# Performance work log

Hardware: AMD Instinct MI355X
Metric: run time of the kernel (lower is better)

The kernel has to match this reference:

```python
import jax, jax.numpy as jnp
import numpy as np

D_MODEL = 1024
D_STATE = 16
D_CONV = 4
D_INNER = 2 * D_MODEL          # expand * d_model
DT_RANK = (D_MODEL + 15) // 16 # ceil(d_model/16) = 64
BATCH, SEQLEN = 2, 1024


def setup_inputs() -> dict:
    key = jax.random.key(0)
    ks = jax.random.split(key, 8)
    s = lambda k, shape, scale=0.02: (jax.random.normal(k, shape, jnp.float32) * scale)
    return {
        "hidden_states": jax.random.normal(ks[0], (BATCH, SEQLEN, D_MODEL), jnp.float32),
        "in_proj_w": s(ks[1], (2 * D_INNER, D_MODEL)),
        "conv_w": s(ks[2], (D_INNER, 1, D_CONV), 0.3),   # depthwise conv kernel (O, I/groups=1, K)
        "conv_b": jnp.zeros((D_INNER,), jnp.float32),
        "x_proj_w": s(ks[3], (DT_RANK + 2 * D_STATE, D_INNER)),
        "dt_proj_w": s(ks[4], (D_INNER, DT_RANK), 0.1),
        # inverse-softplus of small dt values, like the torch init
        "dt_proj_b": jax.random.uniform(ks[5], (D_INNER,), jnp.float32, minval=-5.0, maxval=-2.0),
        "A_log": jnp.log(jnp.broadcast_to(jnp.arange(1, D_STATE + 1, dtype=jnp.float32), (D_INNER, D_STATE))),
        "D": jnp.ones((D_INNER,), jnp.float32),
        "out_proj_w": s(ks[6], (D_MODEL, D_INNER)),
    }


def _forward(hidden_states, in_proj_w, conv_w, conv_b, x_proj_w,
             dt_proj_w, dt_proj_b, A_log, D, out_proj_w):
    B, L, _ = hidden_states.shape
    # in_proj -> split into x, z
    xz = hidden_states @ in_proj_w.T                      # [B, L, 2*d_inner]
    x, z = jnp.split(xz, 2, axis=-1)
    # causal depthwise conv1d (pad left d_conv-1, then take first L) + SiLU
    xc = jnp.transpose(x, (0, 2, 1))                      # [B, d_inner, L]
    xc = jax.lax.conv_general_dilated(
        xc, conv_w, window_strides=(1,), padding=[(D_CONV - 1, 0)],
        feature_group_count=D_INNER,
        dimension_numbers=("NCH", "OIH", "NCH")) + conv_b[None, :, None]
    xc = jax.nn.silu(xc)
    u = jnp.transpose(xc, (0, 2, 1)).astype(jnp.float32)  # [B, L, d_inner]
    # x_proj -> dt_low, B, C
    x_dbl = u @ x_proj_w.T                                # [B, L, dt_rank + 2*d_state]
    dt_low, Bp, Cp = jnp.split(x_dbl, [DT_RANK, DT_RANK + D_STATE], axis=-1)
    dt = dt_low @ dt_proj_w.T + dt_proj_b                 # [B, L, d_inner]
    # NOTE: original adds dt_proj.bias AGAIN as delta_bias inside the scan, then softplus
    delta = jax.nn.softplus(dt + dt_proj_b)
    A = -jnp.exp(A_log.astype(jnp.float32))               # [d_inner, d_state]
    # discretization
    dA = jnp.exp(jnp.einsum("bld,dn->lbdn", delta, A))    # [L, B, d, n]
    dBu = jnp.einsum("bld,bln,bld->lbdn", delta, Bp.astype(jnp.float32), u)
    C_t = jnp.transpose(Cp.astype(jnp.float32), (1, 0, 2))  # [L, B, n]

    def step(state, inp):
        a, b, c = inp
        state = a * state + b                             # [B, d, n]
        y = jnp.einsum("bdn,bn->bd", state, c)
        return state, y

    x0 = jnp.zeros((B, D_INNER, D_STATE), jnp.float32)
    _, ys = jax.lax.scan(step, x0, (dA, dBu, C_t))        # ys: [L, B, d]
    y = jnp.transpose(ys, (1, 0, 2))                      # [B, L, d]
    y = y + u * D.astype(jnp.float32)                     # skip connection
    y = y * jax.nn.silu(z.astype(jnp.float32))            # gating
    y = y.astype(hidden_states.dtype)
    return y @ out_proj_w.T                               # [B, L, d_model]


def reference(hidden_states, in_proj_w, conv_w, conv_b, x_proj_w,
              dt_proj_w, dt_proj_b, A_log, D, out_proj_w):
    return _forward(hidden_states, in_proj_w, conv_w, conv_b, x_proj_w,
                    dt_proj_w, dt_proj_b, A_log, D, out_proj_w)
```

## Files before the change

### kernel.cpp

```cpp
#include <hip/hip_runtime.h>
#include <hip/hip_bf16.h>
#include <math.h>

#define BATCH   2
#define SEQLEN  1024
#define DMODEL  1024
#define DINNER  2048
#define DSTATE  16
#define DTRANK  64
#define XPAD    128
#define MROWS   (BATCH*SEQLEN)
#define NSEG    8
#define SEGLEN  (SEQLEN/NSEG)
#define XP_SPLIT  8

typedef float    f32x4  __attribute__((ext_vector_type(4)));
typedef _Float16 f16x8  __attribute__((ext_vector_type(8)));
typedef _Float16 f16x4  __attribute__((ext_vector_type(4)));

template<int EPI>
__global__ __launch_bounds__(256) void pgemm64(
    const _Float16* __restrict__ A, int lda,
    const _Float16* __restrict__ W, int ldw,
    float* __restrict__ C, int ldc, int K,
    const float* __restrict__ bias, _Float16* __restrict__ C16, size_t zstride)
{
  constexpr int APS = 520;
  constexpr int BPS = 1032;
  __shared__ _Float16 As[2][8 * APS];
  __shared__ _Float16 Bs[2][8 * BPS];

  const int t  = threadIdx.x;
  const int m0 = blockIdx.y * 64, n0 = blockIdx.x * 128;
  const int kchunk = K / gridDim.z;
  const int kbeg = blockIdx.z * kchunk;
  const int nIter = kchunk / 64;

  const int kb = t & 7;
  const int r0 = t >> 3;
  const _Float16* gA = A + (size_t)(m0 + r0) * lda + kbeg + kb * 8;
  const _Float16* gB = W + (size_t)(n0 + r0) * ldw + kbeg + kb * 8;
  const size_t a32 = (size_t)32 * lda;
  const size_t b32 = (size_t)32 * ldw;
  const int aoff = kb * APS + r0 * 8;
  const int boff = kb * BPS + r0 * 8;

  {
    f16x8 a0 = *(const f16x8*)(gA);
    f16x8 a1 = *(const f16x8*)(gA + a32);
    f16x8 b0 = *(const f16x8*)(gB);
    f16x8 b1 = *(const f16x8*)(gB + b32);
    f16x8 b2 = *(const f16x8*)(gB + 2 * b32);
    f16x8 b3 = *(const f16x8*)(gB + 3 * b32);
    gA += 64; gB += 64;
    *(f16x8*)&As[0][aoff]       = a0;
    *(f16x8*)&As[0][aoff + 256] = a1;
    *(f16x8*)&Bs[0][boff]       = b0;
    *(f16x8*)&Bs[0][boff + 256] = b1;
    *(f16x8*)&Bs[0][boff + 512] = b2;
    *(f16x8*)&Bs[0][boff + 768] = b3;
  }

  const int lane = t & 63, wvi = t >> 6;
  const int wn = wvi * 32;
  const int lm = lane & 15, lk = lane >> 4;

  f32x4 acc[4][2] = {};

  for (int it = 0; it < nIter; ++it) {
    __syncthreads();
    const bool more = (it + 1 < nIter);
    f16x8 a0, a1, b0, b1, b2, b3;
    if (more) {
      a0 = *(const f16x8*)(gA);
      a1 = *(const f16x8*)(gA + a32);
      b0 = *(const f16x8*)(gB);
      b1 = *(const f16x8*)(gB + b32);
      b2 = *(const f16x8*)(gB + 2 * b32);
      b3 = *(const f16x8*)(gB + 3 * b32);
      gA += 64; gB += 64;
    }
    const int cb = it & 1;
#pragma unroll
    for (int s = 0; s < 2; ++s) {
      f16x8 av[4], bv[2];
#pragma unroll
      for (int i = 0; i < 4; ++i)
        av[i] = *(const f16x8*)&As[cb][(s * 4 + lk) * APS + (i * 16 + lm) * 8];
#pragma unroll
      for (int j = 0; j < 2; ++j)
        bv[j] = *(const f16x8*)&Bs[cb][(s * 4 + lk) * BPS + (wn + j * 16 + lm) * 8];
#pragma unroll
      for (int i = 0; i < 4; ++i)
#pragma unroll
        for (int j = 0; j < 2; ++j)
          acc[i][j] = __builtin_amdgcn_mfma_f32_16x16x32_f16(av[i], bv[j], acc[i][j], 0, 0, 0);
    }
    if (more) {
      const int nb = (it + 1) & 1;
      *(f16x8*)&As[nb][aoff]       = a0;
      *(f16x8*)&As[nb][aoff + 256] = a1;
      *(f16x8*)&Bs[nb][boff]       = b0;
      *(f16x8*)&Bs[nb][boff + 256] = b1;
      *(f16x8*)&Bs[nb][boff + 512] = b2;
      *(f16x8*)&Bs[nb][boff + 768] = b3;
    }
  }

  float* Cz = C + (size_t)blockIdx.z * zstride;
#pragma unroll
  for (int i = 0; i < 4; ++i) {
    const int mrow = m0 + i * 16 + lk * 4;
#pragma unroll
    for (int j = 0; j < 2; ++j) {
      const int col = n0 + wn + j * 16 + lm;
#pragma unroll
      for (int r = 0; r < 4; ++r) {
        float v = acc[i][j][r];
        size_t off = (size_t)(mrow + r) * ldc + col;
        if constexpr (EPI == 0) {
          Cz[off] = v;
        } else {
          float x = v + 2.f * bias[col];
          float sp = (x > 20.f) ? x : log1pf(__expf(x));
          C16[off] = (_Float16)sp;
        }
      }
    }
  }
}

template<int EPI>
__global__ __launch_bounds__(256) void pgemm128(
    const _Float16* __restrict__ A, int lda,
    const _Float16* __restrict__ W, int ldw,
    float* __restrict__ C, int ldc, int K,
    _Float16* __restrict__ C16)
{
  constexpr int PS = 1032;
  __shared__ _Float16 As[2][8 * PS];
  __shared__ _Float16 Bs[2][8 * PS];

  const int t  = threadIdx.x;
  const int m0 = blockIdx.y * 128, n0 = blockIdx.x * 128;
  const int nIter = K / 64;

  const int kb = t & 7;
  const int r0 = t >> 3;
  const _Float16* gA = A + (size_t)(m0 + r0) * lda + kb * 8;
  const _Float16* gB = W + (size_t)(n0 + r0) * ldw + kb * 8;
  const size_t a32 = (size_t)32 * lda;
  const size_t b32 = (size_t)32 * ldw;
  const int soff = kb * PS + r0 * 8;

  {
    f16x8 ar[4], br[4];
#pragma unroll
    for (int j = 0; j < 4; ++j) {
      ar[j] = *(const f16x8*)(gA + j * a32);
      br[j] = *(const f16x8*)(gB + j * b32);
    }
    gA += 64; gB += 64;
#pragma unroll
    for (int j = 0; j < 4; ++j) {
      *(f16x8*)&As[0][soff + j * 256] = ar[j];
      *(f16x8*)&Bs[0][soff + j * 256] = br[j];
    }
  }

  const int lane = t & 63, wvi = t >> 6;
  const int wm = (wvi >> 1) * 64, wn = (wvi & 1) * 64;
  const int lm = lane & 15, lk = lane >> 4;

  f32x4 acc[4][4] = {};

  for (int it = 0; it < nIter; ++it) {
    __syncthreads();
    const bool more = (it + 1 < nIter);
    f16x8 ar[4], br[4];
    if (more) {
#pragma unroll
      for (int j = 0; j < 4; ++j) {
        ar[j] = *(const f16x8*)(gA + j * a32);
        br[j] = *(const f16x8*)(gB + j * b32);
      }
      gA += 64; gB += 64;
    }
    const int cb = it & 1;
#pragma unroll
    for (int s = 0; s < 2; ++s) {
      f16x8 av[4], bv[4];
#pragma unroll
      for (int i = 0; i < 4; ++i)
        av[i] = *(const f16x8*)&As[cb][(s * 4 + lk) * PS + (wm + i * 16 + lm) * 8];
#pragma unroll
      for (int j = 0; j < 4; ++j)
        bv[j] = *(const f16x8*)&Bs[cb][(s * 4 + lk) * PS + (wn + j * 16 + lm) * 8];
#pragma unroll
      for (int i = 0; i < 4; ++i)
#pragma unroll
        for (int j = 0; j < 4; ++j)
          acc[i][j] = __builtin_amdgcn_mfma_f32_16x16x32_f16(av[i], bv[j], acc[i][j], 0, 0, 0);
    }
    if (more) {
      const int nb = (it + 1) & 1;
#pragma unroll
      for (int j = 0; j < 4; ++j) {
        *(f16x8*)&As[nb][soff + j * 256] = ar[j];
        *(f16x8*)&Bs[nb][soff + j * 256] = br[j];
      }
    }
  }

#pragma unroll
  for (int i = 0; i < 4; ++i) {
    const int mrow = m0 + wm + i * 16 + lk * 4;
#pragma unroll
    for (int j = 0; j < 4; ++j) {
      const int col = n0 + wn + j * 16 + lm;
#pragma unroll
      for (int r = 0; r < 4; ++r) {
        float v = acc[i][j][r];
        size_t off = (size_t)(mrow + r) * ldc + col;
        if constexpr (EPI == 0) {
          C[off] = v;
        } else {
          C16[off] = (_Float16)v;
        }
      }
    }
  }
}

#define R0 (MROWS * DMODEL / 4)
#define R1 (2 * DINNER * DMODEL / 4)
#define R2 (DMODEL * DINNER / 4)
#define R3 (DINNER * DTRANK / 4)
#define R4 (XPAD * DINNER / 4)
#define F2H_TOTAL (R0 + R1 + R2 + R3 + R4)

__global__ __launch_bounds__(256) void f2h_all(
    const float* __restrict__ hid, const float* __restrict__ w_in,
    const float* __restrict__ w_out, const float* __restrict__ w_dt,
    const float* __restrict__ w_xp,
    _Float16* __restrict__ hid16, _Float16* __restrict__ w_in16,
    _Float16* __restrict__ w_out16, _Float16* __restrict__ w_dt16,
    _Float16* __restrict__ w_xp16)
{
  int i = blockIdx.x * 256 + threadIdx.x;
  const float* src; _Float16* dst; int off;
  if (i < R0)                     { src = hid;   dst = hid16;   off = i; }
  else if (i < R0+R1)             { src = w_in;  dst = w_in16;  off = i - R0; }
  else if (i < R0+R1+R2)          { src = w_out; dst = w_out16; off = i - (R0+R1); }
  else if (i < R0+R1+R2+R3)       { src = w_dt;  dst = w_dt16;  off = i - (R0+R1+R2); }
  else if (i < F2H_TOTAL) {
    off = i - (R0+R1+R2+R3);
    int r = (off * 4) >> 11;
    f16x4 h = {0, 0, 0, 0};
    if (r < 96) {
      float4 v = ((const float4*)w_xp)[off];
      h = (f16x4){(_Float16)v.x, (_Float16)v.y, (_Float16)v.z, (_Float16)v.w};
    }
    ((f16x4*)w_xp16)[off] = h;
    return;
  } else return;
  float4 v = ((const float4*)src)[off];
  ((f16x4*)dst)[off] = (f16x4){(_Float16)v.x, (_Float16)v.y, (_Float16)v.z, (_Float16)v.w};
}

__global__ __launch_bounds__(256) void reduce_xdbl(
    const float* __restrict__ part,
    float* __restrict__ xdbl32, _Float16* __restrict__ xdbl16)
{
  int i = blockIdx.x * 256 + threadIdx.x;
  f32x4 s = ((const f32x4*)part)[i];
#pragma unroll
  for (int z = 1; z < XP_SPLIT; ++z)
    s += ((const f32x4*)part)[(size_t)z * (MROWS * XPAD / 4) + i];
  ((f32x4*)xdbl32)[i] = s;
  int col4 = (i & 31) * 4;
  if (col4 < DTRANK) {
    int row = i >> 5;
    *(f16x4*)&xdbl16[(size_t)row * DTRANK + col4] =
        (f16x4){(_Float16)s.x, (_Float16)s.y, (_Float16)s.z, (_Float16)s.w};
  }
}

__global__ __launch_bounds__(256) void conv_silu(
    const _Float16* __restrict__ xz16,
    const float* __restrict__ conv_w,
    const float* __restrict__ conv_b,
    _Float16* __restrict__ u16)
{
  const int idx = blockIdx.x * 256 + threadIdx.x;
  const int d   = idx & (DINNER - 1);
  const int row = idx >> 11;
  const int l   = row & (SEQLEN - 1);
  float s = conv_b[d];
#pragma unroll
  for (int k = 0; k < 4; ++k) {
    int lt = l + k - 3;
    if (lt >= 0)
      s = fmaf((float)xz16[(size_t)(row + k - 3) * (2 * DINNER) + d],
               conv_w[d * 4 + k], s);
  }
  float v = s / (1.f + __expf(-s));
  u16[idx] = (_Float16)v;
}

__device__ __forceinline__ float row_sum16(float x) {
  int v = __builtin_bit_cast(int, x);
  x += __builtin_bit_cast(float, __builtin_amdgcn_update_dpp(0, v, 0x128, 0xF, 0xF, true));
  v = __builtin_bit_cast(int, x);
  x += __builtin_bit_cast(float, __builtin_amdgcn_update_dpp(0, v, 0x124, 0xF, 0xF, true));
  v = __builtin_bit_cast(int, x);
  x += __builtin_bit_cast(float, __builtin_amdgcn_update_dpp(0, v, 0x4E, 0xF, 0xF, true));
  v = __builtin_bit_cast(int, x);
  x += __builtin_bit_cast(float, __builtin_amdgcn_update_dpp(0, v, 0xB1, 0xF, 0xF, true));
  return x;
}

__global__ __launch_bounds__(256) void scan_part1(
    const _Float16* __restrict__ delta16,
    const _Float16* __restrict__ u16,
    const float* __restrict__ x_dbl,
    const float* __restrict__ A_log,
    float* __restrict__ pbuf, float* __restrict__ ebuf)
{
  const int t = threadIdx.x;
  const int c = t >> 4, n = t & 15;
  const int bb = blockIdx.x;
  const int seg = bb >> 8;
  const int r = bb & 255;
  const int b = r >> 7;
  const int d_base = (r & 127) * 16;

  const float A_dn = -__expf(A_log[(d_base + c) * DSTATE + n]);
  float s = 0.f, p = 1.f;

  __shared__ __align__(16) float dl[16 * 68];
  __shared__ __align__(16) float ul[16 * 68];
  __shared__ __align__(16) float Bl[16 * 68];

  const int i_st = t >> 2;
  const int cc = (t & 3) * 4;

  for (int l0 = seg * SEGLEN; l0 < seg * SEGLEN + SEGLEN; l0 += 64) {
    const int row = b * SEQLEN + l0 + i_st;
    {
      f16x4  dh = *(const f16x4*)&delta16[(size_t)row * DINNER + d_base + cc];
      f16x4  uh = *(const f16x4*)&u16[(size_t)row * DINNER + d_base + cc];
      float4 Bv = *(const float4*)&x_dbl[(size_t)row * XPAD + DTRANK + cc];
      dl[(cc+0)*68 + i_st] = (float)dh[0]; dl[(cc+1)*68 + i_st] = (float)dh[1];
      dl[(cc+2)*68 + i_st] = (float)dh[2]; dl[(cc+3)*68 + i_st] = (float)dh[3];
      ul[(cc+0)*68 + i_st] = (float)uh[0]; ul[(cc+1)*68 + i_st] = (float)uh[1];
      ul[(cc+2)*68 + i_st] = (float)uh[2]; ul[(cc+3)*68 + i_st] = (float)uh[3];
      Bl[(cc+0)*68 + i_st] = Bv.x; Bl[(cc+1)*68 + i_st] = Bv.y;
      Bl[(cc+2)*68 + i_st] = Bv.z; Bl[(cc+3)*68 + i_st] = Bv.w;
    }
    __syncthreads();
#pragma unroll
    for (int i0 = 0; i0 < 64; i0 += 4) {
      f32x4 dv4 = *(const f32x4*)&dl[c * 68 + i0];
      f32x4 uv4 = *(const f32x4*)&ul[c * 68 + i0];
      f32x4 Bv4 = *(const f32x4*)&Bl[n * 68 + i0];
#pragma unroll
      for (int rr = 0; rr < 4; ++rr) {
        float dA = __expf(dv4[rr] * A_dn);
        s = fmaf(dA, s, dv4[rr] * Bv4[rr] * uv4[rr]);
        p *= dA;
      }
    }
    __syncthreads();
  }
  const int peIdx = (r * NSEG + seg) * 256 + t;
  pbuf[peIdx] = p;
  ebuf[peIdx] = s;
}

__global__ __launch_bounds__(256) void scan_part2(
    const _Float16* __restrict__ delta16,
    const _Float16* __restrict__ u16,
    const _Float16* __restrict__ xz16,
    const float* __restrict__ x_dbl,
    const float* __restrict__ A_log,
    const float* __restrict__ Dp,
    const float* __restrict__ pbuf,
    const float* __restrict__ ebuf,
    _Float16* __restrict__ y16)
{
  const int t = threadIdx.x;
  const int c = t >> 4, n = t & 15;
  const int bb = blockIdx.x;
  const int seg = bb >> 8;
  const int r = bb & 255;
  const int b = r >> 7;
  const int d_base = (r & 127) * 16;

  const float A_dn = -__expf(A_log[(d_base + c) * DSTATE + n]);

  float s = 0.f;
  {
    const int base = r * NSEG * 256 + t;
    for (int k = 0; k < seg; ++k)
      s = fmaf(pbuf[base + k * 256], s, ebuf[base + k * 256]);
  }

  __shared__ __align__(16) float dl[16 * 68];
  __shared__ __align__(16) float ul[16 * 68];
  __shared__ __align__(16) float Bl[16 * 68];
  __shared__ __align__(16) float Cl[16 * 68];
  __shared__ __align__(16) float yl[16 * 68];
  __shared__ __align__(16) float z_s[64 * 16];
  __shared__ float Dp_s[16];

  if (t < 16) Dp_s[t] = Dp[d_base + t];

  const int i_st = t >> 2;
  const int cc = (t & 3) * 4;

  for (int l0 = seg * SEGLEN; l0 < seg * SEGLEN + SEGLEN; l0 += 64) {
    const int row = b * SEQLEN + l0 + i_st;
    {
      f16x4  dh = *(const f16x4*)&delta16[(size_t)row * DINNER + d_base + cc];
      f16x4  uh = *(const f16x4*)&u16[(size_t)row * DINNER + d_base + cc];
      float4 Bv = *(const float4*)&x_dbl[(size_t)row * XPAD + DTRANK + cc];
      float4 Cv = *(const float4*)&x_dbl[(size_t)row * XPAD + DTRANK + DSTATE + cc];
      f16x4  zh = *(const f16x4*)&xz16[(size_t)row * (2 * DINNER) + DINNER + d_base + cc];
      dl[(cc+0)*68 + i_st] = (float)dh[0]; dl[(cc+1)*68 + i_st] = (float)dh[1];
      dl[(cc+2)*68 + i_st] = (float)dh[2]; dl[(cc+3)*68 + i_st] = (float)dh[3];
      ul[(cc+0)*68 + i_st] = (float)uh[0]; ul[(cc+1)*68 + i_st] = (float)uh[1];
      ul[(cc+2)*68 + i_st] = (float)uh[2]; ul[(cc+3)*68 + i_st] = (float)uh[3];
      Bl[(cc+0)*68 + i_st] = Bv.x; Bl[(cc+1)*68 + i_st] = Bv.y;
      Bl[(cc+2)*68 + i_st] = Bv.z; Bl[(cc+3)*68 + i_st] = Bv.w;
      Cl[(cc+0)*68 + i_st] = Cv.x; Cl[(cc+1)*68 + i_st] = Cv.y;
      Cl[(cc+2)*68 + i_st] = Cv.z; Cl[(cc+3)*68 + i_st] = Cv.w;
      float4 zv = make_float4((float)zh[0], (float)zh[1], (float)zh[2], (float)zh[3]);
      *(float4*)&z_s[t * 4] = zv;
    }
    __syncthreads();

#pragma unroll
    for (int i0 = 0; i0 < 64; i0 += 4) {
      f32x4 dv4 = *(const f32x4*)&dl[c * 68 + i0];
      f32x4 uv4 = *(const f32x4*)&ul[c * 68 + i0];
      f32x4 Bv4 = *(const f32x4*)&Bl[n * 68 + i0];
      f32x4 Cv4 = *(const f32x4*)&Cl[n * 68 + i0];
      f32x4 py;
#pragma unroll
      for (int rr = 0; rr < 4; ++rr) {
        float dA = __expf(dv4[rr] * A_dn);
        s = fmaf(dA, s, dv4[rr] * Bv4[rr] * uv4[rr]);
        py[rr] = row_sum16(s * Cv4[rr]);
      }
      if (n == 0) *(f32x4*)&yl[c * 68 + i0] = py;
    }
    __syncthreads();

#pragma unroll
    for (int k = 0; k < 4; ++k) {
      int o = t + 256 * k;
      int i = o >> 4, c2 = o & 15;
      float ssum = yl[c2 * 68 + i];
      float uv = ul[c2 * 68 + i];
      float zv = z_s[o];
      float yv = fmaf(uv, Dp_s[c2], ssum);
      yv *= zv / (1.f + __expf(-zv));
      y16[(size_t)(b * SEQLEN + l0 + i) * DINNER + d_base + c2] = (_Float16)yv;
    }
    __syncthreads();
  }
}

extern "C" void kernel_launch(void* const* d_in, const int* in_sizes, int n_in,
                              void* d_out, int out_size, void* d_ws, size_t ws_size,
                              hipStream_t stream)
{
  const float* hidden     = (const float*)d_in[0];
  const float* in_proj_w  = (const float*)d_in[1];
  const float* conv_w     = (const float*)d_in[2];
  const float* conv_b     = (const float*)d_in[3];
  const float* x_proj_w   = (const float*)d_in[4];
  const float* dt_proj_w  = (const float*)d_in[5];
  const float* dt_proj_b  = (const float*)d_in[6];
  const float* A_log      = (const float*)d_in[7];
  const float* Dp         = (const float*)d_in[8];
  const float* out_proj_w = (const float*)d_in[9];
  float* out = (float*)d_out;

  char* p = (char*)d_ws;
  _Float16* xz16    = (_Float16*)p;  p += (size_t)MROWS * 2 * DINNER * 2;
  _Float16* u16     = (_Float16*)p;  p += (size_t)MROWS * DINNER * 2;
  float*    xdbl32  = (float*)p;     p += (size_t)MROWS * XPAD * 4;
  _Float16* delta16 = (_Float16*)p;  p += (size_t)MROWS * DINNER * 2;
  _Float16* h16     = (_Float16*)p;  p += (size_t)MROWS * DMODEL * 2;
  _Float16* win16   = (_Float16*)p;  p += (size_t)2 * DINNER * DMODEL * 2;
  _Float16* wout16  = (_Float16*)p;  p += (size_t)DMODEL * DINNER * 2;
  _Float16* wdt16   = (_Float16*)p;  p += (size_t)DINNER * DTRANK * 2;
  _Float16* wxp16   = (_Float16*)p;  p += (size_t)XPAD * DINNER * 2;
  _Float16* xdbl16  = (_Float16*)p;  p += (size_t)MROWS * DTRANK * 2;
  _Float16* y16     = (_Float16*)p;  p += (size_t)MROWS * DINNER * 2;
  float*    pbuf    = (float*)p;     p += (size_t)256 * NSEG * 256 * 4;
  float*    ebuf    = (float*)p;     p += (size_t)256 * NSEG * 256 * 4;
  float*    xp_part = (float*)delta16;

  f2h_all<<<(F2H_TOTAL + 255) / 256, 256, 0, stream>>>(
      hidden, in_proj_w, out_proj_w, dt_proj_w, x_proj_w,
      h16, win16, wout16, wdt16, wxp16);

  pgemm128<4><<<dim3(4096 / 128, MROWS / 128, 1), 256, 0, stream>>>(
      h16, DMODEL, win16, DMODEL, nullptr, 4096, DMODEL, xz16);

  conv_silu<<<(MROWS * DINNER) / 256, 256, 0, stream>>>(xz16, conv_w, conv_b, u16);

  pgemm64<0><<<dim3(1, MROWS / 64, XP_SPLIT), 256, 0, stream>>>(
      u16, DINNER, wxp16, DINNER, xp_part, XPAD, DINNER, nullptr, nullptr,
      (size_t)MROWS * XPAD);

  reduce_xdbl<<<(MROWS * XPAD / 4) / 256, 256, 0, stream>>>(xp_part, xdbl32, xdbl16);

  pgemm64<2><<<dim3(DINNER / 128, MROWS / 64, 1), 256, 0, stream>>>(
      xdbl16, DTRANK, wdt16, DTRANK, nullptr, DINNER, DTRANK, dt_proj_b, delta16, 0);

  scan_part1<<<256 * NSEG, 256, 0, stream>>>(delta16, u16, xdbl32, A_log, pbuf, ebuf);
  scan_part2<<<256 * NSEG, 256, 0, stream>>>(delta16, u16, xz16, xdbl32, A_log, Dp,
                                             pbuf, ebuf, y16);

  pgemm64<0><<<dim3(DMODEL / 128, MROWS / 64, 1), 256, 0, stream>>>(
      y16, DINNER, wout16, DINNER, out, DMODEL, DINNER, nullptr, nullptr, 0);
}
```

Before: 244.1 us.

## Fuse causal conv and SiLU into x_proj GEMM and scan loaders

Removes the standalone conv_silu kernel and the u16 intermediate buffer. The depthwise causal conv plus SiLU is now recomputed from xz16 inside the x_proj GEMM's A-tile loader and inside both scan kernels' shared-memory staging. This saves one launch and a write and reread of an 8 MB activation. In exchange, each consumer reads four shifted rows of xz16 and recomputes exp, so global reads and ALU work triple, and the GEMM's A loads become slower.

After: 255.7 us. +4.8%, slower.

```diff
diff --git a/kernel.cpp b/kernel.cpp
--- a/kernel.cpp
+++ b/kernel.cpp
@@ -18,12 +18,40 @@
 typedef _Float16 f16x8  __attribute__((ext_vector_type(8)));
 typedef _Float16 f16x4  __attribute__((ext_vector_type(4)));
 
-template<int EPI>
+__device__ __forceinline__ f16x8 conv_row8(
+    const _Float16* __restrict__ xz, int mrow, int dbase,
+    const float* __restrict__ conv_w, const float* __restrict__ conv_b)
+{
+  const int l = mrow & (SEQLEN - 1);
+  const _Float16* base = xz + (size_t)mrow * (2 * DINNER) + dbase;
+  float acc[8];
+#pragma unroll
+  for (int j = 0; j < 8; ++j) acc[j] = conv_b[dbase + j];
+#pragma unroll
+  for (int k = 0; k < 4; ++k) {
+    if (l + k - 3 >= 0) {
+      f16x8 xh = *(const f16x8*)(base + (ptrdiff_t)(k - 3) * (2 * DINNER));
+#pragma unroll
+      for (int j = 0; j < 8; ++j)
+        acc[j] = fmaf((float)xh[j], conv_w[(dbase + j) * 4 + k], acc[j]);
+    }
+  }
+  f16x8 r;
+#pragma unroll
+  for (int j = 0; j < 8; ++j) {
+    float s = acc[j];
+    r[j] = (_Float16)(s / (1.f + __expf(-s)));
+  }
+  return r;
+}
+
+template<int EPI, bool CONVA>
 __global__ __launch_bounds__(256) void pgemm64(
     const _Float16* __restrict__ A, int lda,
     const _Float16* __restrict__ W, int ldw,
     float* __restrict__ C, int ldc, int K,
-    const float* __restrict__ bias, _Float16* __restrict__ C16, size_t zstride)
+    const float* __restrict__ bias, _Float16* __restrict__ C16, size_t zstride,
+    const float* __restrict__ conv_w, const float* __restrict__ conv_b)
 {
   constexpr int APS = 520;
   constexpr int BPS = 1032;
@@ -44,15 +72,22 @@
   const size_t b32 = (size_t)32 * ldw;
   const int aoff = kb * APS + r0 * 8;
   const int boff = kb * BPS + r0 * 8;
+  int kcur = kbeg;
 
   {
-    f16x8 a0 = *(const f16x8*)(gA);
-    f16x8 a1 = *(const f16x8*)(gA + a32);
+    f16x8 a0, a1;
+    if constexpr (CONVA) {
+      a0 = conv_row8(A, m0 + r0,      kcur + kb * 8, conv_w, conv_b);
+      a1 = conv_row8(A, m0 + r0 + 32, kcur + kb * 8, conv_w, conv_b);
+    } else {
+      a0 = *(const f16x8*)(gA);
+      a1 = *(const f16x8*)(gA + a32);
+    }
     f16x8 b0 = *(const f16x8*)(gB);
     f16x8 b1 = *(const f16x8*)(gB + b32);
     f16x8 b2 = *(const f16x8*)(gB + 2 * b32);
     f16x8 b3 = *(const f16x8*)(gB + 3 * b32);
-    gA += 64; gB += 64;
+    gA += 64; gB += 64; kcur += 64;
     *(f16x8*)&As[0][aoff]       = a0;
     *(f16x8*)&As[0][aoff + 256] = a1;
     *(f16x8*)&Bs[0][boff]       = b0;
@@ -72,13 +107,18 @@
     const bool more = (it + 1 < nIter);
     f16x8 a0, a1, b0, b1, b2, b3;
     if (more) {
-      a0 = *(const f16x8*)(gA);
-      a1 = *(const f16x8*)(gA + a32);
+      if constexpr (CONVA) {
+        a0 = conv_row8(A, m0 + r0,      kcur + kb * 8, conv_w, conv_b);
+        a1 = conv_row8(A, m0 + r0 + 32, kcur + kb * 8, conv_w, conv_b);
+      } else {
+        a0 = *(const f16x8*)(gA);
+        a1 = *(const f16x8*)(gA + a32);
+      }
       b0 = *(const f16x8*)(gB);
       b1 = *(const f16x8*)(gB + b32);
       b2 = *(const f16x8*)(gB + 2 * b32);
       b3 = *(const f16x8*)(gB + 3 * b32);
-      gA += 64; gB += 64;
+      gA += 64; gB += 64; kcur += 64;
     }
     const int cb = it & 1;
 #pragma unroll
@@ -286,28 +326,6 @@
   }
 }
 
-__global__ __launch_bounds__(256) void conv_silu(
-    const _Float16* __restrict__ xz16,
-    const float* __restrict__ conv_w,
-    const float* __restrict__ conv_b,
-    _Float16* __restrict__ u16)
-{
-  const int idx = blockIdx.x * 256 + threadIdx.x;
-  const int d   = idx & (DINNER - 1);
-  const int row = idx >> 11;
-  const int l   = row & (SEQLEN - 1);
-  float s = conv_b[d];
-#pragma unroll
-  for (int k = 0; k < 4; ++k) {
-    int lt = l + k - 3;
-    if (lt >= 0)
-      s = fmaf((float)xz16[(size_t)(row + k - 3) * (2 * DINNER) + d],
-               conv_w[d * 4 + k], s);
-  }
-  float v = s / (1.f + __expf(-s));
-  u16[idx] = (_Float16)v;
-}
-
 __device__ __forceinline__ float row_sum16(float x) {
   int v = __builtin_bit_cast(int, x);
   x += __builtin_bit_cast(float, __builtin_amdgcn_update_dpp(0, v, 0x128, 0xF, 0xF, true));
@@ -322,9 +340,11 @@
 
 __global__ __launch_bounds__(256) void scan_part1(
     const _Float16* __restrict__ delta16,
-    const _Float16* __restrict__ u16,
+    const _Float16* __restrict__ xz16,
     const float* __restrict__ x_dbl,
     const float* __restrict__ A_log,
+    const float* __restrict__ conv_w,
+    const float* __restrict__ conv_b,
     float* __restrict__ pbuf, float* __restrict__ ebuf)
 {
   const int t = threadIdx.x;
@@ -345,16 +365,36 @@
   const int i_st = t >> 2;
   const int cc = (t & 3) * 4;
 
+  float cw[4][4], cb4[4];
+#pragma unroll
+  for (int j = 0; j < 4; ++j) {
+    cb4[j] = conv_b[d_base + cc + j];
+#pragma unroll
+    for (int k = 0; k < 4; ++k) cw[j][k] = conv_w[(d_base + cc + j) * 4 + k];
+  }
+
   for (int l0 = seg * SEGLEN; l0 < seg * SEGLEN + SEGLEN; l0 += 64) {
     const int row = b * SEQLEN + l0 + i_st;
+    const int l = l0 + i_st;
     {
       f16x4  dh = *(const f16x4*)&delta16[(size_t)row * DINNER + d_base + cc];
-      f16x4  uh = *(const f16x4*)&u16[(size_t)row * DINNER + d_base + cc];
       float4 Bv = *(const float4*)&x_dbl[(size_t)row * XPAD + DTRANK + cc];
+      float ua[4] = {cb4[0], cb4[1], cb4[2], cb4[3]};
+#pragma unroll
+      for (int k = 0; k < 4; ++k) {
+        if (l + k - 3 >= 0) {
+          f16x4 xh = *(const f16x4*)&xz16[(size_t)(row + k - 3) * (2 * DINNER) + d_base + cc];
+#pragma unroll
+          for (int j = 0; j < 4; ++j) ua[j] = fmaf((float)xh[j], cw[j][k], ua[j]);
+        }
+      }
       dl[(cc+0)*68 + i_st] = (float)dh[0]; dl[(cc+1)*68 + i_st] = (float)dh[1];
       dl[(cc+2)*68 + i_st] = (float)dh[2]; dl[(cc+3)*68 + i_st] = (float)dh[3];
-      ul[(cc+0)*68 + i_st] = (float)uh[0]; ul[(cc+1)*68 + i_st] = (float)uh[1];
-      ul[(cc+2)*68 + i_st] = (float)uh[2]; ul[(cc+3)*68 + i_st] = (float)uh[3];
+#pragma unroll
+      for (int j = 0; j < 4; ++j) {
+        float us = ua[j];
+        ul[(cc+j)*68 + i_st] = us / (1.f + __expf(-us));
+      }
       Bl[(cc+0)*68 + i_st] = Bv.x; Bl[(cc+1)*68 + i_st] = Bv.y;
       Bl[(cc+2)*68 + i_st] = Bv.z; Bl[(cc+3)*68 + i_st] = Bv.w;
     }
@@ -380,11 +420,12 @@
 
 __global__ __launch_bounds__(256) void scan_part2(
     const _Float16* __restrict__ delta16,
-    const _Float16* __restrict__ u16,
     const _Float16* __restrict__ xz16,
     const float* __restrict__ x_dbl,
     const float* __restrict__ A_log,
     const float* __restrict__ Dp,
+    const float* __restrict__ conv_w,
+    const float* __restrict__ conv_b,
     const float* __restrict__ pbuf,
     const float* __restrict__ ebuf,
     _Float16* __restrict__ y16)
@@ -419,18 +460,38 @@
   const int i_st = t >> 2;
   const int cc = (t & 3) * 4;
 
+  float cw[4][4], cb4[4];
+#pragma unroll
+  for (int j = 0; j < 4; ++j) {
+    cb4[j] = conv_b[d_base + cc + j];
+#pragma unroll
+    for (int k = 0; k < 4; ++k) cw[j][k] = conv_w[(d_base + cc + j) * 4 + k];
+  }
+
   for (int l0 = seg * SEGLEN; l0 < seg * SEGLEN + SEGLEN; l0 += 64) {
     const int row = b * SEQLEN + l0 + i_st;
+    const int l = l0 + i_st;
     {
       f16x4  dh = *(const f16x4*)&delta16[(size_t)row * DINNER + d_base + cc];
-      f16x4  uh = *(const f16x4*)&u16[(size_t)row * DINNER + d_base + cc];
       float4 Bv = *(const float4*)&x_dbl[(size_t)row * XPAD + DTRANK + cc];
       float4 Cv = *(const float4*)&x_dbl[(size_t)row * XPAD + DTRANK + DSTATE + cc];
       f16x4  zh = *(const f16x4*)&xz16[(size_t)row * (2 * DINNER) + DINNER + d_base + cc];
+      float ua[4] = {cb4[0], cb4[1], cb4[2], cb4[3]};
+#pragma unroll
+      for (int k = 0; k < 4; ++k) {
+        if (l + k - 3 >= 0) {
+          f16x4 xh = *(const f16x4*)&xz16[(size_t)(row + k - 3) * (2 * DINNER) + d_base + cc];
+#pragma unroll
+          for (int j = 0; j < 4; ++j) ua[j] = fmaf((float)xh[j], cw[j][k], ua[j]);
+        }
+      }
       dl[(cc+0)*68 + i_st] = (float)dh[0]; dl[(cc+1)*68 + i_st] = (float)dh[1];
       dl[(cc+2)*68 + i_st] = (float)dh[2]; dl[(cc+3)*68 + i_st] = (float)dh[3];
-      ul[(cc+0)*68 + i_st] = (float)uh[0]; ul[(cc+1)*68 + i_st] = (float)uh[1];
-      ul[(cc+2)*68 + i_st] = (float)uh[2]; ul[(cc+3)*68 + i_st] = (float)uh[3];
+#pragma unroll
+      for (int j = 0; j < 4; ++j) {
+        float us = ua[j];
+        ul[(cc+j)*68 + i_st] = us / (1.f + __expf(-us));
+      }
       Bl[(cc+0)*68 + i_st] = Bv.x; Bl[(cc+1)*68 + i_st] = Bv.y;
       Bl[(cc+2)*68 + i_st] = Bv.z; Bl[(cc+3)*68 + i_st] = Bv.w;
       Cl[(cc+0)*68 + i_st] = Cv.x; Cl[(cc+1)*68 + i_st] = Cv.y;
@@ -490,7 +551,6 @@
 
   char* p = (char*)d_ws;
   _Float16* xz16    = (_Float16*)p;  p += (size_t)MROWS * 2 * DINNER * 2;
-  _Float16* u16     = (_Float16*)p;  p += (size_t)MROWS * DINNER * 2;
   float*    xdbl32  = (float*)p;     p += (size_t)MROWS * XPAD * 4;
   _Float16* delta16 = (_Float16*)p;  p += (size_t)MROWS * DINNER * 2;
   _Float16* h16     = (_Float16*)p;  p += (size_t)MROWS * DMODEL * 2;
@@ -511,21 +571,22 @@
   pgemm128<4><<<dim3(4096 / 128, MROWS / 128, 1), 256, 0, stream>>>(
       h16, DMODEL, win16, DMODEL, nullptr, 4096, DMODEL, xz16);
 
-  conv_silu<<<(MROWS * DINNER) / 256, 256, 0, stream>>>(xz16, conv_w, conv_b, u16);
-
-  pgemm64<0><<<dim3(1, MROWS / 64, XP_SPLIT), 256, 0, stream>>>(
-      u16, DINNER, wxp16, DINNER, xp_part, XPAD, DINNER, nullptr, nullptr,
-      (size_t)MROWS * XPAD);
+  pgemm64<0, true><<<dim3(1, MROWS / 64, XP_SPLIT), 256, 0, stream>>>(
+      xz16, 2 * DINNER, wxp16, DINNER, xp_part, XPAD, DINNER,
+      nullptr, nullptr, (size_t)MROWS * XPAD, conv_w, conv_b);
 
   reduce_xdbl<<<(MROWS * XPAD / 4) / 256, 256, 0, stream>>>(xp_part, xdbl32, xdbl16);
 
-  pgemm64<2><<<dim3(DINNER / 128, MROWS / 64, 1), 256, 0, stream>>>(
-      xdbl16, DTRANK, wdt16, DTRANK, nullptr, DINNER, DTRANK, dt_proj_b, delta16, 0);
-
-  scan_part1<<<256 * NSEG, 256, 0, stream>>>(delta16, u16, xdbl32, A_log, pbuf, ebuf);
-  scan_part2<<<256 * NSEG, 256, 0, stream>>>(delta16, u16, xz16, xdbl32, A_log, Dp,
-                                             pbuf, ebuf, y16);
-
-  pgemm64<0><<<dim3(DMODEL / 128, MROWS / 64, 1), 256, 0, stream>>>(
-      y16, DINNER, wout16, DINNER, out, DMODEL, DINNER, nullptr, nullptr, 0);
-}
+  pgemm64<2, false><<<dim3(DINNER / 128, MROWS / 64, 1), 256, 0, stream>>>(
+      xdbl16, DTRANK, wdt16, DTRANK, nullptr, DINNER, DTRANK,
+      dt_proj_b, delta16, 0, nullptr, nullptr);
+
+  scan_part1<<<256 * NSEG, 256, 0, stream>>>(delta16, xz16, xdbl32, A_log,
+                                             conv_w, conv_b, pbuf, ebuf);
+  scan_part2<<<256 * NSEG, 256, 0, stream>>>(delta16, xz16, xdbl32, A_log, Dp,
+                                             conv_w, conv_b, pbuf, ebuf, y16);
+
+  pgemm64<0, false><<<dim3(DMODEL / 128, MROWS / 64, 1), 256, 0, stream>>>(
+      y16, DINNER, wout16, DINNER, out, DMODEL, DINNER,
+      nullptr, nullptr, 0, nullptr, nullptr);
+}
```
